# Kernel optimization log

Hardware: AMD Instinct MI355X
Metric: run time of the kernel (lower is better)

Reference implementation:

```python
import jax, jax.numpy as jnp
import numpy as np

D = 768; NH = 12; HD = D // NH; L = 12; NC = 27; PATCH = 16; MLP = 3072; PROJ = 512
IMG = 224; GRID = IMG // PATCH; HW = GRID * GRID; S = NC + HW
NEG = -1e9

def _ln(x, w, b):
    m = jnp.mean(x, -1, keepdims=True)
    v = jnp.mean(jnp.square(x - m), -1, keepdims=True)
    return (x - m) * jax.lax.rsqrt(v + 1e-5) * w + b

def _quick_gelu(x):
    return x * jax.nn.sigmoid(1.702 * x)

def _build_mask(attn_obj_masks, dtype):
    # CRIS block mask: cls<->cls blocked except self; cls->patch allowed only for
    # patches of that class; patch->cls blocked; patch->patch fully allowed.
    B = attn_obj_masks.shape[0]
    oh = jax.nn.one_hot(attn_obj_masks, NC, dtype=dtype)              # [B, HW, NC]
    T11 = jnp.broadcast_to(1.0 - jnp.eye(NC, dtype=dtype), (B, NC, NC))
    M13 = 1.0 - jnp.swapaxes(oh, 1, 2)                                # [B, NC, HW]
    top = jnp.concatenate([T11, M13], axis=2)
    bot = jnp.concatenate([jnp.ones((B, HW, NC), dtype), jnp.zeros((B, HW, HW), dtype)], axis=2)
    Mb = jnp.concatenate([top, bot], axis=1)                          # [B, S, S]
    return jnp.where(Mb == 1.0, jnp.asarray(NEG, dtype), jnp.asarray(0.0, dtype))

def reference(img, sents, attn_obj_masks, obj_masks, cls_tokens, patch_w, patch_b, pos_embed,
              ln1_w, ln1_b, qkv_w, qkv_b, out_w, out_b, ln2_w, ln2_b,
              mlp_w1, mlp_b1, mlp_w2, mlp_b2, ln_post_w, ln_post_b, proj):
    B = img.shape[0]
    sents = sents / jnp.linalg.norm(sents, axis=-1, keepdims=True)    # encode_text output, L2 normed
    mask = _build_mask(attn_obj_masks, img.dtype)                     # [B, S, S]
    # patch embedding (conv stride 16) -> [B, HW, D]
    p = jax.lax.conv_general_dilated(img, patch_w, (PATCH, PATCH), 'VALID',
                                     dimension_numbers=('NCHW', 'OIHW', 'NCHW'))
    p = p.reshape(B, D, HW).transpose(0, 2, 1) + patch_b
    x = jnp.concatenate([jnp.broadcast_to(cls_tokens, (B, NC, D)), p], axis=1) + pos_embed
    scale = 1.0 / np.sqrt(HD).astype(np.float32)
    def block(x, prm):
        l1w, l1b, qw, qb, ow, ob, l2w, l2b, w1, b1, w2, b2 = prm
        h = _ln(x, l1w, l1b)
        qkv = h @ qw + qb
        q, k, v = jnp.split(qkv, 3, axis=-1)
        q = q.reshape(B, S, NH, HD).transpose(0, 2, 1, 3)
        k = k.reshape(B, S, NH, HD).transpose(0, 2, 1, 3)
        v = v.reshape(B, S, NH, HD).transpose(0, 2, 1, 3)
        scores = jnp.einsum('bhqd,bhkd->bhqk', q, k) * scale + mask[:, None]
        a = jax.nn.softmax(scores, axis=-1)
        o = jnp.einsum('bhqk,bhkd->bhqd', a, v).transpose(0, 2, 1, 3).reshape(B, S, D)
        x = x + o @ ow + ob
        h = _ln(x, l2w, l2b)
        x = x + _quick_gelu(h @ w1 + b1) @ w2 + b2
        return x, None
    x, _ = jax.lax.scan(block, x, (ln1_w, ln1_b, qkv_w, qkv_b, out_w, out_b,
                                   ln2_w, ln2_b, mlp_w1, mlp_b1, mlp_w2, mlp_b2))
    tokens = _ln(x, ln_post_w, ln_post_b) @ proj                      # [B, S, PROJ]
    obj = tokens[:, :NC]
    obj = obj / jnp.linalg.norm(obj, axis=-1, keepdims=True)
    pred_id = jnp.einsum('bnd,bd->bn', obj, sents)                    # [B, NC]
    # per-class scatter loop == gather of pred_id by per-pixel class id
    pred = jnp.take_along_axis(pred_id, obj_masks.reshape(B, -1), axis=1).reshape(obj_masks.shape)
    return pred                                                       # [B, 224, 224]

def setup_inputs():
    B = 16; std = 0.02
    ks = jax.random.split(jax.random.key(0), 16)
    f = jax.random.normal
    return {
        'img': f(ks[0], (B, 3, IMG, IMG), jnp.float32),
        'sents': f(ks[1], (B, PROJ), jnp.float32),
        'attn_obj_masks': jax.random.randint(ks[2], (B, HW), 0, NC, jnp.int32),
        'obj_masks': jax.random.randint(ks[3], (B, IMG, IMG), 0, NC, jnp.int32),
        'cls_tokens': f(ks[4], (1, NC, D)) * std,
        'patch_w': f(ks[5], (D, 3, PATCH, PATCH)) * std,
        'patch_b': jnp.zeros((D,)),
        'pos_embed': f(ks[6], (S, D)) * std,
        'ln1_w': jnp.ones((L, D)), 'ln1_b': jnp.zeros((L, D)),
        'qkv_w': f(ks[7], (L, D, 3 * D)) * std, 'qkv_b': jnp.zeros((L, 3 * D)),
        'out_w': f(ks[8], (L, D, D)) * std, 'out_b': jnp.zeros((L, D)),
        'ln2_w': jnp.ones((L, D)), 'ln2_b': jnp.zeros((L, D)),
        'mlp_w1': f(ks[9], (L, D, MLP)) * std, 'mlp_b1': jnp.zeros((L, MLP)),
        'mlp_w2': f(ks[10], (L, MLP, D)) * std, 'mlp_b2': jnp.zeros((L, D)),
        'ln_post_w': jnp.ones((D,)), 'ln_post_b': jnp.zeros((D,)),
        'proj': f(ks[11], (D, PROJ)) * std,
    }
```

## Files before the change

kernel.cpp:

```cpp
#include <hip/hip_runtime.h>

#define DEV __device__ __forceinline__

typedef short bf16x8 __attribute__((ext_vector_type(8)));
typedef float f32x4 __attribute__((ext_vector_type(4)));
typedef int vi4 __attribute__((ext_vector_type(4)));
typedef unsigned short u16;

#define NEGV -1000000000.0f

DEV u16 f2bf(float f) {
  union { float f; unsigned u; } v; v.f = f;
  unsigned r = v.u + 0x7FFFu + ((v.u >> 16) & 1u);
  return (u16)(r >> 16);
}

DEV bf16x8 ld_bf8(const u16* p) {
  vi4 v = *(const vi4*)p;
  return __builtin_bit_cast(bf16x8, v);
}

DEV void gload_lds16(const u16* g, vi4* l) {
  __builtin_amdgcn_global_load_lds((const __attribute__((address_space(1))) void*)g,
                                   (__attribute__((address_space(3))) void*)l, 16, 0, 0);
}

template<int BN, int MODE, bool GELU, int KS>
__global__ __launch_bounds__(256) void gemm_bt(
    const u16* __restrict__ A, const u16* __restrict__ Bt,
    const float* __restrict__ bias,
    float* __restrict__ Cf, u16* __restrict__ Cb,
    int M, int N, int K, const float* __restrict__ pos)
{
  constexpr int FJ = BN / 32;
  constexpr int LB = BN / 64;
  constexpr int LTOT = 2 + LB;
  __shared__ vi4 As[3][512];
  __shared__ vi4 Bs[3][BN * 4];

  int gx = gridDim.x, gy = gridDim.y;
  int nwg = gx * gy * (int)gridDim.z;
  int orig = blockIdx.x + gx * (blockIdx.y + gy * blockIdx.z);
  int qq = nwg >> 3, rr = nwg & 7;
  int xcd = orig & 7, off = orig >> 3;
  int id = (xcd < rr) ? xcd * (qq + 1) + off : rr * (qq + 1) + (xcd - rr) * qq + off;
  int bx = id % gx, rest = id / gx, by = rest % gy, bz = rest / gy;

  int tid = threadIdx.x, lane = tid & 63, wid = tid >> 6;
  int wm = wid >> 1, wn = wid & 1;
  int m0 = by * 128, n0 = bx * BN;
  int kBeg = (K / KS) * bz;
  int nT = (K / KS) >> 5;
  f32x4 acc[4][FJ] = {};

  auto STAGE = [&](int buf, int kk) {
    #pragma unroll
    for (int r = 0; r < 2; ++r) {
      int flat = r * 256 + tid;
      int row = flat >> 2, c = flat & 3;
      int cs = c ^ ((row >> 1) & 3);
      gload_lds16(A + (long)(m0 + row) * K + kk + cs * 8, &As[buf][r * 256 + wid * 64]);
    }
    #pragma unroll
    for (int r = 0; r < LB; ++r) {
      int flat = r * 256 + tid;
      int row = flat >> 2, c = flat & 3;
      int cs = c ^ ((row >> 1) & 3);
      gload_lds16(Bt + (long)(n0 + row) * K + kk + cs * 8, &Bs[buf][r * 256 + wid * 64]);
    }
  };

  STAGE(0, kBeg);
  STAGE(1, kBeg + 32);
  int cur = 0;
  for (int t = 0; t < nT; ++t) {
    int kk = kBeg + t * 32;
    if (t + 2 < nT) {
      STAGE((t + 2) % 3, kk + 64);
      asm volatile("s_waitcnt vmcnt(%0)" :: "i"(2 * LTOT) : "memory");
    } else if (t + 1 < nT) {
      asm volatile("s_waitcnt vmcnt(%0)" :: "i"(LTOT) : "memory");
    } else {
      asm volatile("s_waitcnt vmcnt(0)" ::: "memory");
    }
    __builtin_amdgcn_s_barrier();
    bf16x8 af[4], bfr[FJ];
    int cg = lane >> 4, l15 = lane & 15;
    #pragma unroll
    for (int i = 0; i < 4; ++i) {
      int ra = wm * 64 + i * 16 + l15;
      af[i] = __builtin_bit_cast(bf16x8, As[cur][ra * 4 + (cg ^ ((ra >> 1) & 3))]);
    }
    #pragma unroll
    for (int j = 0; j < FJ; ++j) {
      int rb = wn * (BN / 2) + j * 16 + l15;
      bfr[j] = __builtin_bit_cast(bf16x8, Bs[cur][rb * 4 + (cg ^ ((rb >> 1) & 3))]);
    }
    #pragma unroll
    for (int i = 0; i < 4; ++i)
      #pragma unroll
      for (int j = 0; j < FJ; ++j)
        acc[i][j] = __builtin_amdgcn_mfma_f32_16x16x32_bf16(af[i], bfr[j], acc[i][j], 0, 0, 0);
    __builtin_amdgcn_s_barrier();
    cur = (cur + 1) % 3;
  }

  int cg = lane >> 4, l15 = lane & 15;
  #pragma unroll
  for (int i = 0; i < 4; ++i) {
    #pragma unroll
    for (int j = 0; j < FJ; ++j) {
      int col = n0 + wn * (BN / 2) + j * 16 + l15;
      float bv = bias ? bias[col] : 0.f;
      #pragma unroll
      for (int r = 0; r < 4; ++r) {
        int row = m0 + wm * 64 + i * 16 + cg * 4 + r;
        if (row < M) {
          float v = acc[i][j][r];
          if (KS == 1 || bz == 0) v += bv;
          if (GELU) v = v / (1.f + __expf(-1.702f * v));
          if (MODE == 0) Cb[(long)row * N + col] = f2bf(v);
          else if (MODE == 1) {
            if (KS > 1) atomicAdd(&Cf[(long)row * N + col], v);
            else Cf[(long)row * N + col] += v;
          }
          else if (MODE == 2) Cf[(long)row * N + col] = v;
          else {
            int hw = row % 196;
            int xr = (row / 196) * 223 + 27 + hw;
            Cf[(long)xr * 768 + col] = v + pos[(27 + hw) * 768 + col];
          }
        }
      }
    }
  }
}

__global__ __launch_bounds__(256) void attn_kernel(
    const u16* __restrict__ QKV, const int* __restrict__ aom, u16* __restrict__ O)
{
  __shared__ vi4 Kl[224 * 8];
  __shared__ vi4 Vt[64 * 28];
  __shared__ vi4 Pl[4][16 * 28];
  __shared__ int ml[196];
  int tid = threadIdx.x, lane = tid & 63, wid = tid >> 6;
  int qg = blockIdx.x, h = blockIdx.y, b = blockIdx.z;
  long rowbase = (long)b * 223;
  #pragma unroll
  for (int it = 0; it < 7; ++it) {
    int flat = it * 256 + tid;
    int s = flat >> 3, c = flat & 7;
    int cs = c ^ (s & 7);
    gload_lds16(QKV + (rowbase + s) * 2304 + 768 + h * 64 + cs * 8, &Kl[it * 256 + wid * 64]);
  }
  u16* vt16 = (u16*)Vt;
  #pragma unroll
  for (int it = 0; it < 7; ++it) {
    int flat = it * 256 + tid;
    int s = flat >> 3, c = flat & 7;
    vi4 v = {0, 0, 0, 0};
    if (s < 223) v = *(const vi4*)(QKV + (rowbase + s) * 2304 + 1536 + h * 64 + c * 8);
    union { vi4 v4; u16 hx[8]; } uu; uu.v4 = v;
    int cs = s >> 3;
    #pragma unroll
    for (int j = 0; j < 8; ++j) {
      int d = c * 8 + j;
      vt16[d * 224 + (cs ^ ((d >> 1) & 3)) * 8 + (s & 7)] = uu.hx[j];
    }
  }
  for (int i = tid; i < 196; i += 256) ml[i] = aom[b * 196 + i];
  __syncthreads();

  int colk = lane & 15, cg = lane >> 4;
  #pragma unroll
  for (int rep = 0; rep < 2; ++rep) {
    int fo = wid * 2 + rep;
    if (fo >= 7) break;
    int qf = qg * 7 + fo;
    int q0 = qf * 16;
    int arow = q0 + colk; if (arow > 222) arow = 222;
    const u16* qb = QKV + (rowbase + arow) * 2304 + h * 64;
    bf16x8 aq0 = ld_bf8(qb + cg * 8);
    bf16x8 aq1 = ld_bf8(qb + 32 + cg * 8);

    f32x4 sc[14];
    #pragma unroll
    for (int kf = 0; kf < 14; ++kf) {
      int key = kf * 16 + colk;
      f32x4 a = {0.f, 0.f, 0.f, 0.f};
      bf16x8 bk0 = __builtin_bit_cast(bf16x8, Kl[key * 8 + (cg ^ (key & 7))]);
      bf16x8 bk1 = __builtin_bit_cast(bf16x8, Kl[key * 8 + ((4 + cg) ^ (key & 7))]);
      a = __builtin_amdgcn_mfma_f32_16x16x32_bf16(aq0, bk0, a, 0, 0, 0);
      a = __builtin_amdgcn_mfma_f32_16x16x32_bf16(aq1, bk1, a, 0, 0, 0);
      sc[kf] = a;
    }
    #pragma unroll
    for (int r = 0; r < 4; ++r) {
      int q = q0 + cg * 4 + r;
      float mx = -3.4e38f;
      #pragma unroll
      for (int kf = 0; kf < 14; ++kf) {
        int key = kf * 16 + colk;
        float mval;
        if (key >= 223) mval = NEGV;
        else if (q >= 27) mval = (key < 27) ? NEGV : 0.f;
        else if (key < 27) mval = (key == q) ? 0.f : NEGV;
        else mval = (ml[key - 27] == q) ? 0.f : NEGV;
        float s = sc[kf][r] * 0.125f + mval;
        sc[kf][r] = s;
        mx = fmaxf(mx, s);
      }
      #pragma unroll
      for (int d = 1; d < 16; d <<= 1) mx = fmaxf(mx, __shfl_xor(mx, d));
      float sum = 0.f;
      #pragma unroll
      for (int kf = 0; kf < 14; ++kf) {
        float e = __expf(sc[kf][r] - mx);
        sc[kf][r] = e; sum += e;
      }
      #pragma unroll
      for (int d = 1; d < 16; d <<= 1) sum += __shfl_xor(sum, d);
      float inv = 1.f / sum;
      #pragma unroll
      for (int kf = 0; kf < 14; ++kf) sc[kf][r] *= inv;
    }
    u16* pw = (u16*)Pl[wid];
    #pragma unroll
    for (int kf = 0; kf < 14; ++kf) {
      int key = kf * 16 + colk;
      int ck = key >> 3;
      #pragma unroll
      for (int r = 0; r < 4; ++r) {
        int prow = cg * 4 + r;
        pw[prow * 224 + (ck ^ ((prow >> 1) & 3)) * 8 + (key & 7)] = f2bf(sc[kf][r]);
      }
    }
    f32x4 oacc[4] = {};
    #pragma unroll
    for (int ks = 0; ks < 7; ++ks) {
      bf16x8 pa = __builtin_bit_cast(bf16x8, Pl[wid][colk * 28 + ((ks * 4 + cg) ^ ((colk >> 1) & 3))]);
      #pragma unroll
      for (int nf = 0; nf < 4; ++nf) {
        int d = nf * 16 + colk;
        bf16x8 bv = __builtin_bit_cast(bf16x8, Vt[d * 28 + ((ks * 4 + cg) ^ ((d >> 1) & 3))]);
        oacc[nf] = __builtin_amdgcn_mfma_f32_16x16x32_bf16(pa, bv, oacc[nf], 0, 0, 0);
      }
    }
    #pragma unroll
    for (int nf = 0; nf < 4; ++nf) {
      int d = h * 64 + nf * 16 + colk;
      #pragma unroll
      for (int r = 0; r < 4; ++r) {
        int q = q0 + cg * 4 + r;
        if (q < 223) O[(rowbase + q) * 768 + d] = f2bf(oacc[nf][r]);
      }
    }
  }
}

template<bool MAP27>
__global__ __launch_bounds__(256) void ln_kernel(
    const float* __restrict__ X, u16* __restrict__ Hb,
    const float* __restrict__ w, const float* __restrict__ bb)
{
  __shared__ float sb[8];
  int r = blockIdx.x;
  int xr = MAP27 ? (r / 27) * 223 + (r % 27) : r;
  const float* xp = X + (long)xr * 768;
  int t = threadIdx.x;
  float v0 = xp[t], v1 = xp[t + 256], v2 = xp[t + 512];
  float s = v0 + v1 + v2;
  #pragma unroll
  for (int d = 1; d < 64; d <<= 1) s += __shfl_xor(s, d);
  if ((t & 63) == 0) sb[t >> 6] = s;
  __syncthreads();
  float mean = (sb[0] + sb[1] + sb[2] + sb[3]) * (1.f / 768.f);
  float d0 = v0 - mean, d1 = v1 - mean, d2 = v2 - mean;
  float q = d0 * d0 + d1 * d1 + d2 * d2;
  #pragma unroll
  for (int d = 1; d < 64; d <<= 1) q += __shfl_xor(q, d);
  if ((t & 63) == 0) sb[4 + (t >> 6)] = q;
  __syncthreads();
  float var = (sb[4] + sb[5] + sb[6] + sb[7]) * (1.f / 768.f);
  float rs = rsqrtf(var + 1e-5f);
  Hb[(long)r * 768 + t]       = f2bf(d0 * rs * w[t] + bb[t]);
  Hb[(long)r * 768 + t + 256] = f2bf(d1 * rs * w[t + 256] + bb[t + 256]);
  Hb[(long)r * 768 + t + 512] = f2bf(d2 * rs * w[t + 512] + bb[t + 512]);
}

__global__ __launch_bounds__(256) void transpose_w(
    const float* __restrict__ W, u16* __restrict__ WT, int K, int N, long sW, long sT)
{
  __shared__ float t[64][65];
  int z = blockIdx.z;
  W += (long)z * sW; WT += (long)z * sT;
  int n0 = blockIdx.x * 64, k0 = blockIdx.y * 64;
  #pragma unroll
  for (int i = 0; i < 4; ++i) {
    int flat = i * 256 + threadIdx.x;
    int r = flat >> 4, c = (flat & 15) * 4;
    float4 v = *(const float4*)(W + (long)(k0 + r) * N + n0 + c);
    t[r][c] = v.x; t[r][c + 1] = v.y; t[r][c + 2] = v.z; t[r][c + 3] = v.w;
  }
  __syncthreads();
  #pragma unroll
  for (int i = 0; i < 8; ++i) {
    int flat = i * 256 + threadIdx.x;
    int rn = flat >> 5, ck = (flat & 31) * 2;
    unsigned val = (unsigned)f2bf(t[ck][rn]) | ((unsigned)f2bf(t[ck + 1][rn]) << 16);
    *(unsigned*)(WT + (long)(n0 + rn) * K + k0 + ck) = val;
  }
}

__global__ void convert_bf16(const float* __restrict__ src, u16* __restrict__ dst, int n) {
  int i = blockIdx.x * 256 + threadIdx.x;
  if (i < n) dst[i] = f2bf(src[i]);
}

__global__ __launch_bounds__(256) void patch_extract(const float* __restrict__ img, u16* __restrict__ Xp) {
  int row = blockIdx.x;
  int b = row / 196, hw = row % 196, gh = hw / 14, gw = hw % 14;
  for (int idx = threadIdx.x; idx < 768; idx += 256) {
    int cch = idx >> 8, rem = idx & 255, kh = rem >> 4, kw = rem & 15;
    Xp[(long)row * 768 + idx] = f2bf(img[((long)(b * 3 + cch) * 224 + gh * 16 + kh) * 224 + gw * 16 + kw]);
  }
}

__global__ void cls_pos_fill(const float* __restrict__ cls, const float* __restrict__ pos, float* __restrict__ x) {
  int i = blockIdx.x * 256 + threadIdx.x;
  if (i >= 16 * 27 * 768) return;
  int d = i % 768, t = i / 768, b = t / 27, s = t % 27;
  x[((long)b * 223 + s) * 768 + d] = cls[s * 768 + d] + pos[s * 768 + d];
}

__global__ __launch_bounds__(256) void sents_norm(const float* __restrict__ s, float* __restrict__ sn) {
  __shared__ float sb[4];
  int b = blockIdx.x, t = threadIdx.x;
  float v0 = s[b * 512 + t], v1 = s[b * 512 + t + 256];
  float q = v0 * v0 + v1 * v1;
  #pragma unroll
  for (int d = 1; d < 64; d <<= 1) q += __shfl_xor(q, d);
  if ((t & 63) == 0) sb[t >> 6] = q;
  __syncthreads();
  float inv = rsqrtf(sb[0] + sb[1] + sb[2] + sb[3]);
  sn[b * 512 + t] = v0 * inv;
  sn[b * 512 + t + 256] = v1 * inv;
}

__global__ __launch_bounds__(256) void obj_dot(const float* __restrict__ obj, const float* __restrict__ sn, float* __restrict__ pid) {
  __shared__ float sb[8];
  int r = blockIdx.x, t = threadIdx.x, b = r / 27;
  float v0 = obj[(long)r * 512 + t], v1 = obj[(long)r * 512 + t + 256];
  float w0 = sn[b * 512 + t], w1 = sn[b * 512 + t + 256];
  float q = v0 * v0 + v1 * v1;
  float dt = v0 * w0 + v1 * w1;
  #pragma unroll
  for (int d = 1; d < 64; d <<= 1) { q += __shfl_xor(q, d); dt += __shfl_xor(dt, d); }
  if ((t & 63) == 0) { sb[t >> 6] = q; sb[4 + (t >> 6)] = dt; }
  __syncthreads();
  if (t == 0) pid[r] = (sb[4] + sb[5] + sb[6] + sb[7]) * rsqrtf(sb[0] + sb[1] + sb[2] + sb[3]);
}

__global__ void gather_pred(const int* __restrict__ om, const float* __restrict__ pid, float* __restrict__ out) {
  int i = blockIdx.x * 256 + threadIdx.x;
  if (i >= 16 * 224 * 224) return;
  int b = i / (224 * 224);
  out[i] = pid[b * 27 + om[i]];
}

extern "C" void kernel_launch(void* const* d_in, const int* in_sizes, int n_in,
                              void* d_out, int out_size, void* d_ws, size_t ws_size,
                              hipStream_t stream) {
  const float* img     = (const float*)d_in[0];
  const float* sents   = (const float*)d_in[1];
  const int*   aom     = (const int*)d_in[2];
  const int*   omask   = (const int*)d_in[3];
  const float* cls     = (const float*)d_in[4];
  const float* patch_w = (const float*)d_in[5];
  const float* patch_b = (const float*)d_in[6];
  const float* pos     = (const float*)d_in[7];
  const float* ln1w    = (const float*)d_in[8];
  const float* ln1b    = (const float*)d_in[9];
  const float* qkvw    = (const float*)d_in[10];
  const float* qkvb    = (const float*)d_in[11];
  const float* outw    = (const float*)d_in[12];
  const float* outb    = (const float*)d_in[13];
  const float* ln2w    = (const float*)d_in[14];
  const float* ln2b    = (const float*)d_in[15];
  const float* m1w     = (const float*)d_in[16];
  const float* m1b     = (const float*)d_in[17];
  const float* m2w     = (const float*)d_in[18];
  const float* m2b     = (const float*)d_in[19];
  const float* lnpw    = (const float*)d_in[20];
  const float* lnpb    = (const float*)d_in[21];
  const float* projw   = (const float*)d_in[22];

  char* p = (char*)d_ws;
  auto alloc = [&](size_t bytes) { char* r = p; p += (bytes + 255) & ~(size_t)255; return r; };
  float* x   = (float*)alloc(3568ul * 768 * 4);
  u16* H     = (u16*)alloc(3584ul * 768 * 2);
  u16* QKV   = (u16*)alloc(3584ul * 2304 * 2);
  u16* Obuf  = (u16*)alloc(3584ul * 768 * 2);
  u16* G     = (u16*)alloc(3584ul * 3072 * 2);
  u16* PWc   = (u16*)alloc(768ul * 768 * 2);
  u16* PrT   = (u16*)alloc(512ul * 768 * 2);
  float* obj = (float*)alloc(432ul * 512 * 4);
  float* sn  = (float*)alloc(16ul * 512 * 4);
  float* pid = (float*)alloc(432ul * 4);

  const size_t wlayer = (2304ul * 768 + 768ul * 768 + 3072ul * 768 + 768ul * 3072) * 2;
  size_t used = (size_t)(p - (char*)d_ws);
  int nw = (ws_size >= used + 12 * wlayer + 65536) ? 12 : 1;
  const long sQ = 2304l * 768, sO = 768l * 768, s1 = 768l * 3072, s2 = 3072l * 768;
  u16* WqT = (u16*)alloc((size_t)sQ * 2 * nw);
  u16* WoT = (u16*)alloc((size_t)sO * 2 * nw);
  u16* W1T = (u16*)alloc((size_t)s1 * 2 * nw);
  u16* W2T = (u16*)alloc((size_t)s2 * 2 * nw);

  convert_bf16<<<2304, 256, 0, stream>>>(patch_w, PWc, 768 * 768);
  transpose_w<<<dim3(8, 12, 1), 256, 0, stream>>>(projw, PrT, 768, 512, 0, 0);
  if (nw == 12) {
    transpose_w<<<dim3(36, 12, 12), 256, 0, stream>>>(qkvw, WqT, 768, 2304, sQ, sQ);
    transpose_w<<<dim3(12, 12, 12), 256, 0, stream>>>(outw, WoT, 768, 768, sO, sO);
    transpose_w<<<dim3(48, 12, 12), 256, 0, stream>>>(m1w, W1T, 768, 3072, s1, s1);
    transpose_w<<<dim3(12, 48, 12), 256, 0, stream>>>(m2w, W2T, 3072, 768, s2, s2);
  }
  patch_extract<<<3136, 256, 0, stream>>>(img, H);
  cls_pos_fill<<<1296, 256, 0, stream>>>(cls, pos, x);
  gemm_bt<64, 3, false, 1><<<dim3(12, 25), 256, 0, stream>>>(H, PWc, patch_b, x, nullptr, 3136, 768, 768, pos);

  for (int l = 0; l < 12; ++l) {
    u16 *wq, *wo, *w1, *w2;
    if (nw == 12) { wq = WqT + (long)l * sQ; wo = WoT + (long)l * sO; w1 = W1T + (long)l * s1; w2 = W2T + (long)l * s2; }
    else {
      wq = WqT; wo = WoT; w1 = W1T; w2 = W2T;
      transpose_w<<<dim3(36, 12, 1), 256, 0, stream>>>(qkvw + (long)l * sQ, wq, 768, 2304, 0, 0);
      transpose_w<<<dim3(12, 12, 1), 256, 0, stream>>>(outw + (long)l * sO, wo, 768, 768, 0, 0);
      transpose_w<<<dim3(48, 12, 1), 256, 0, stream>>>(m1w + (long)l * s1, w1, 768, 3072, 0, 0);
      transpose_w<<<dim3(12, 48, 1), 256, 0, stream>>>(m2w + (long)l * s2, w2, 3072, 768, 0, 0);
    }
    ln_kernel<false><<<3568, 256, 0, stream>>>(x, H, ln1w + l * 768, ln1b + l * 768);
    gemm_bt<128, 0, false, 1><<<dim3(18, 28), 256, 0, stream>>>(H, wq, qkvb + l * 2304, nullptr, QKV, 3568, 2304, 768, nullptr);
    attn_kernel<<<dim3(2, 12, 16), 256, 0, stream>>>(QKV, aom, Obuf);
    gemm_bt<64, 1, false, 2><<<dim3(12, 28, 2), 256, 0, stream>>>(Obuf, wo, outb + l * 768, x, nullptr, 3568, 768, 768, nullptr);
    ln_kernel<false><<<3568, 256, 0, stream>>>(x, H, ln2w + l * 768, ln2b + l * 768);
    gemm_bt<128, 0, true, 1><<<dim3(24, 28), 256, 0, stream>>>(H, w1, m1b + l * 3072, nullptr, G, 3568, 3072, 768, nullptr);
    gemm_bt<64, 1, false, 2><<<dim3(12, 28, 2), 256, 0, stream>>>(G, w2, m2b + l * 768, x, nullptr, 3568, 768, 3072, nullptr);
  }

  ln_kernel<true><<<432, 256, 0, stream>>>(x, H, lnpw, lnpb);
  gemm_bt<64, 2, false, 1><<<dim3(8, 4), 256, 0, stream>>>(H, PrT, nullptr, obj, nullptr, 432, 512, 768, nullptr);
  sents_norm<<<16, 256, 0, stream>>>(sents, sn);
  obj_dot<<<432, 256, 0, stream>>>(obj, sn, pid);
  gather_pred<<<3136, 256, 0, stream>>>(omask, pid, (float*)d_out);
}
```

Baseline: 2.440 ms.

## Use double-buffered GEMM, narrower QKV/MLP1 tiles, and warp-per-row LayerNorm

The GEMM pipeline drops from triple to double buffering, prefetching one stage ahead instead of two, which shrinks LDS use and may let more workgroups fit per CU. The QKV and MLP-up GEMMs switch from 128-wide to 64-wide N tiles, doubling the grid to improve load balance and occupancy at the cost of more A-tile reloads. LayerNorm is rewritten so each 64-lane wavefront handles one row with float4 loads, shuffle-only reductions and vectorized bf16 stores, removing shared memory and block barriers. The shallower prefetch may expose more global-load latency in the GEMM main loop.

```diff
diff --git a/kernel.cpp b/kernel.cpp
--- a/kernel.cpp
+++ b/kernel.cpp
@@ -6,6 +6,7 @@
 typedef float f32x4 __attribute__((ext_vector_type(4)));
 typedef int vi4 __attribute__((ext_vector_type(4)));
 typedef unsigned short u16;
+typedef short short4v __attribute__((ext_vector_type(4)));
 
 #define NEGV -1000000000.0f
 
@@ -35,8 +36,8 @@
   constexpr int FJ = BN / 32;
   constexpr int LB = BN / 64;
   constexpr int LTOT = 2 + LB;
-  __shared__ vi4 As[3][512];
-  __shared__ vi4 Bs[3][BN * 4];
+  __shared__ vi4 As[2][512];
+  __shared__ vi4 Bs[2][BN * 4];
 
   int gx = gridDim.x, gy = gridDim.y;
   int nwg = gx * gy * (int)gridDim.z;
@@ -49,8 +50,7 @@
   int tid = threadIdx.x, lane = tid & 63, wid = tid >> 6;
   int wm = wid >> 1, wn = wid & 1;
   int m0 = by * 128, n0 = bx * BN;
-  int kBeg = (K / KS) * bz;
-  int nT = (K / KS) >> 5;
+  int kBeg = (K / KS) * bz, kEnd = kBeg + K / KS;
   f32x4 acc[4][FJ] = {};
 
   auto STAGE = [&](int buf, int kk) {
@@ -71,14 +71,10 @@
   };
 
   STAGE(0, kBeg);
-  STAGE(1, kBeg + 32);
   int cur = 0;
-  for (int t = 0; t < nT; ++t) {
-    int kk = kBeg + t * 32;
-    if (t + 2 < nT) {
-      STAGE((t + 2) % 3, kk + 64);
-      asm volatile("s_waitcnt vmcnt(%0)" :: "i"(2 * LTOT) : "memory");
-    } else if (t + 1 < nT) {
+  for (int kk = kBeg; kk < kEnd; kk += 32) {
+    if (kk + 32 < kEnd) {
+      STAGE(cur ^ 1, kk + 32);
       asm volatile("s_waitcnt vmcnt(%0)" :: "i"(LTOT) : "memory");
     } else {
       asm volatile("s_waitcnt vmcnt(0)" ::: "memory");
@@ -102,7 +98,7 @@
       for (int j = 0; j < FJ; ++j)
         acc[i][j] = __builtin_amdgcn_mfma_f32_16x16x32_bf16(af[i], bfr[j], acc[i][j], 0, 0, 0);
     __builtin_amdgcn_s_barrier();
-    cur = (cur + 1) % 3;
+    cur ^= 1;
   }
 
   int cg = lane >> 4, l15 = lane & 15;
@@ -261,31 +257,42 @@
 template<bool MAP27>
 __global__ __launch_bounds__(256) void ln_kernel(
     const float* __restrict__ X, u16* __restrict__ Hb,
-    const float* __restrict__ w, const float* __restrict__ bb)
+    const float* __restrict__ w, const float* __restrict__ bb, int nrows)
 {
-  __shared__ float sb[8];
-  int r = blockIdx.x;
-  int xr = MAP27 ? (r / 27) * 223 + (r % 27) : r;
-  const float* xp = X + (long)xr * 768;
-  int t = threadIdx.x;
-  float v0 = xp[t], v1 = xp[t + 256], v2 = xp[t + 512];
-  float s = v0 + v1 + v2;
-  #pragma unroll
-  for (int d = 1; d < 64; d <<= 1) s += __shfl_xor(s, d);
-  if ((t & 63) == 0) sb[t >> 6] = s;
-  __syncthreads();
-  float mean = (sb[0] + sb[1] + sb[2] + sb[3]) * (1.f / 768.f);
-  float d0 = v0 - mean, d1 = v1 - mean, d2 = v2 - mean;
-  float q = d0 * d0 + d1 * d1 + d2 * d2;
-  #pragma unroll
-  for (int d = 1; d < 64; d <<= 1) q += __shfl_xor(q, d);
-  if ((t & 63) == 0) sb[4 + (t >> 6)] = q;
-  __syncthreads();
-  float var = (sb[4] + sb[5] + sb[6] + sb[7]) * (1.f / 768.f);
-  float rs = rsqrtf(var + 1e-5f);
-  Hb[(long)r * 768 + t]       = f2bf(d0 * rs * w[t] + bb[t]);
-  Hb[(long)r * 768 + t + 256] = f2bf(d1 * rs * w[t + 256] + bb[t + 256]);
-  Hb[(long)r * 768 + t + 512] = f2bf(d2 * rs * w[t + 512] + bb[t + 512]);
+  int row = blockIdx.x * 4 + (threadIdx.x >> 6);
+  if (row >= nrows) return;
+  int xr = MAP27 ? (row / 27) * 223 + (row % 27) : row;
+  int l = threadIdx.x & 63;
+  const float4* xp = (const float4*)(X + (long)xr * 768);
+  float4 a = xp[l], c = xp[l + 64], d = xp[l + 128];
+  float s = a.x + a.y + a.z + a.w + c.x + c.y + c.z + c.w + d.x + d.y + d.z + d.w;
+  #pragma unroll
+  for (int t = 1; t < 64; t <<= 1) s += __shfl_xor(s, t);
+  float mean = s * (1.f / 768.f);
+  a.x -= mean; a.y -= mean; a.z -= mean; a.w -= mean;
+  c.x -= mean; c.y -= mean; c.z -= mean; c.w -= mean;
+  d.x -= mean; d.y -= mean; d.z -= mean; d.w -= mean;
+  float q = a.x*a.x + a.y*a.y + a.z*a.z + a.w*a.w
+          + c.x*c.x + c.y*c.y + c.z*c.z + c.w*c.w
+          + d.x*d.x + d.y*d.y + d.z*d.z + d.w*d.w;
+  #pragma unroll
+  for (int t = 1; t < 64; t <<= 1) q += __shfl_xor(q, t);
+  float rs = rsqrtf(q * (1.f / 768.f) + 1e-5f);
+  const float4* wp = (const float4*)w;
+  const float4* bp = (const float4*)bb;
+  u16* out = Hb + (long)row * 768;
+  float4 w0 = wp[l], w1 = wp[l + 64], w2 = wp[l + 128];
+  float4 b0 = bp[l], b1 = bp[l + 64], b2 = bp[l + 128];
+  short4v o;
+  o[0] = (short)f2bf(a.x * rs * w0.x + b0.x); o[1] = (short)f2bf(a.y * rs * w0.y + b0.y);
+  o[2] = (short)f2bf(a.z * rs * w0.z + b0.z); o[3] = (short)f2bf(a.w * rs * w0.w + b0.w);
+  *(short4v*)(out + l * 4) = o;
+  o[0] = (short)f2bf(c.x * rs * w1.x + b1.x); o[1] = (short)f2bf(c.y * rs * w1.y + b1.y);
+  o[2] = (short)f2bf(c.z * rs * w1.z + b1.z); o[3] = (short)f2bf(c.w * rs * w1.w + b1.w);
+  *(short4v*)(out + 256 + l * 4) = o;
+  o[0] = (short)f2bf(d.x * rs * w2.x + b2.x); o[1] = (short)f2bf(d.y * rs * w2.y + b2.y);
+  o[2] = (short)f2bf(d.z * rs * w2.z + b2.z); o[3] = (short)f2bf(d.w * rs * w2.w + b2.w);
+  *(short4v*)(out + 512 + l * 4) = o;
 }
 
 __global__ __launch_bounds__(256) void transpose_w(
@@ -439,16 +446,16 @@
       transpose_w<<<dim3(48, 12, 1), 256, 0, stream>>>(m1w + (long)l * s1, w1, 768, 3072, 0, 0);
       transpose_w<<<dim3(12, 48, 1), 256, 0, stream>>>(m2w + (long)l * s2, w2, 3072, 768, 0, 0);
     }
-    ln_kernel<false><<<3568, 256, 0, stream>>>(x, H, ln1w + l * 768, ln1b + l * 768);
-    gemm_bt<128, 0, false, 1><<<dim3(18, 28), 256, 0, stream>>>(H, wq, qkvb + l * 2304, nullptr, QKV, 3568, 2304, 768, nullptr);
+    ln_kernel<false><<<892, 256, 0, stream>>>(x, H, ln1w + l * 768, ln1b + l * 768, 3568);
+    gemm_bt<64, 0, false, 1><<<dim3(36, 28), 256, 0, stream>>>(H, wq, qkvb + l * 2304, nullptr, QKV, 3568, 2304, 768, nullptr);
     attn_kernel<<<dim3(2, 12, 16), 256, 0, stream>>>(QKV, aom, Obuf);
     gemm_bt<64, 1, false, 2><<<dim3(12, 28, 2), 256, 0, stream>>>(Obuf, wo, outb + l * 768, x, nullptr, 3568, 768, 768, nullptr);
-    ln_kernel<false><<<3568, 256, 0, stream>>>(x, H, ln2w + l * 768, ln2b + l * 768);
-    gemm_bt<128, 0, true, 1><<<dim3(24, 28), 256, 0, stream>>>(H, w1, m1b + l * 3072, nullptr, G, 3568, 3072, 768, nullptr);
+    ln_kernel<false><<<892, 256, 0, stream>>>(x, H, ln2w + l * 768, ln2b + l * 768, 3568);
+    gemm_bt<64, 0, true, 1><<<dim3(48, 28), 256, 0, stream>>>(H, w1, m1b + l * 3072, nullptr, G, 3568, 3072, 768, nullptr);
     gemm_bt<64, 1, false, 2><<<dim3(12, 28, 2), 256, 0, stream>>>(G, w2, m2b + l * 768, x, nullptr, 3568, 768, 3072, nullptr);
   }
 
-  ln_kernel<true><<<432, 256, 0, stream>>>(x, H, lnpw, lnpb);
+  ln_kernel<true><<<108, 256, 0, stream>>>(x, H, lnpw, lnpb, 432);
   gemm_bt<64, 2, false, 1><<<dim3(8, 4), 256, 0, stream>>>(H, PrT, nullptr, obj, nullptr, 432, 512, 768, nullptr);
   sents_norm<<<16, 256, 0, stream>>>(sents, sn);
   obj_dot<<<432, 256, 0, stream>>>(obj, sn, pid);
```

Measured after the change: 2.497 ms. +2.3%, slower.
